# Optimization experiments

Measured on AMD Instinct MI355X. Metric: run time of the kernel, lower is better.

The kernel has to match this reference:

```python
import jax, jax.numpy as jnp
import numpy as np

VX = 1.0 / 3.2
VY = 1.0 / 3.2
X_MIN, Y_MIN = -40.0, -20.0
NX, NY = 256, 256  # grid: (40-(-40))/VX, (60-(-20))/VY
X_OFF = VX / 2.0 + X_MIN
Y_OFF = VY / 2.0 + Y_MIN


def setup_inputs() -> dict:
    key = jax.random.key(0)
    ks = jax.random.split(key, 14)
    B = 8
    Ma, Pa, Ca = 60000, 20, 5
    Mr, Pr, Cr = 80000, 32, 3
    Da, Dr, Co = 64, 64, 32
    voxels_agent = jax.random.normal(ks[0], (Ma, Pa, Ca), jnp.float32)
    coors_agent = jnp.stack([
        jax.random.randint(ks[1], (Ma,), 0, B),
        jax.random.randint(ks[2], (Ma,), 0, NY),
        jax.random.randint(ks[3], (Ma,), 0, NX)], axis=-1).astype(jnp.int32)
    num_points_agent = jax.random.randint(ks[4], (Ma,), 1, Pa + 1).astype(jnp.int32)
    voxels_rg = jax.random.normal(ks[5], (Mr, Pr, Cr), jnp.float32)
    coors_rg = jnp.stack([
        jax.random.randint(ks[6], (Mr,), 0, B),
        jax.random.randint(ks[7], (Mr,), 0, NY),
        jax.random.randint(ks[8], (Mr,), 0, NX)], axis=-1).astype(jnp.int32)
    num_points_rg = jax.random.randint(ks[9], (Mr,), 1, Pr + 1).astype(jnp.int32)
    w_agent = 0.02 * jax.random.normal(ks[10], (Ca + 5, Da), jnp.float32)
    b_agent = jnp.zeros((Da,), jnp.float32)
    w_rg = 0.02 * jax.random.normal(ks[11], (Cr + 5, Dr), jnp.float32)
    b_rg = jnp.zeros((Dr,), jnp.float32)
    conv_w = 0.02 * jax.random.normal(ks[12], (3, 3, Da + Dr, Co), jnp.float32)
    conv_b = jnp.zeros((Co,), jnp.float32)
    return dict(voxels_agent=voxels_agent, coors_agent=coors_agent,
                num_points_agent=num_points_agent, voxels_rg=voxels_rg,
                coors_rg=coors_rg, num_points_rg=num_points_rg,
                w_agent=w_agent, b_agent=b_agent, w_rg=w_rg, b_rg=b_rg,
                conv_w=conv_w, conv_b=conv_b, batch_size=B)


def _pillar_vfe(voxels, coors, num_points, W, b):
    # voxels [M,P,C]; coors [M,3]=(batch,y,x); num_points [M]
    M, P, C = voxels.shape
    mask = (jnp.arange(P)[None, :] < num_points[:, None]).astype(voxels.dtype)[..., None]  # [M,P,1]
    npts = jnp.maximum(num_points, 1).astype(voxels.dtype)[:, None, None]
    xyz = voxels[..., :3]
    mean = jnp.sum(xyz * mask, axis=1, keepdims=True) / npts          # pillar cluster mean
    f_cluster = xyz - mean                                            # [M,P,3]
    cx = coors[:, 2].astype(voxels.dtype)[:, None]
    cy = coors[:, 1].astype(voxels.dtype)[:, None]
    f_cx = voxels[..., 0] - (cx * VX + X_OFF)                         # offset from pillar center
    f_cy = voxels[..., 1] - (cy * VY + Y_OFF)
    feats = jnp.concatenate([voxels, f_cluster,
                             jnp.stack([f_cx, f_cy], axis=-1)], axis=-1) * mask  # [M,P,C+5]
    h = jax.nn.relu(feats @ W + b)                                    # [M,P,D]
    return jnp.max(h * mask, axis=1)                                  # [M,D]


def _scatter(feats, coors, B):
    # scatter pillar features into dense BEV canvas [B,NY,NX,D]
    D = feats.shape[1]
    idx = coors[:, 0] * (NY * NX) + coors[:, 1] * NX + coors[:, 2]
    canvas = jnp.zeros((B * NY * NX, D), feats.dtype).at[idx].set(feats)
    return canvas.reshape(B, NY, NX, D)


def reference(voxels_agent, coors_agent, num_points_agent, voxels_rg, coors_rg,
              num_points_rg, w_agent, b_agent, w_rg, b_rg, conv_w, conv_b,
              batch_size):
    pa = _pillar_vfe(voxels_agent, coors_agent, num_points_agent, w_agent, b_agent)
    ca = _scatter(pa, coors_agent, batch_size)
    pr = _pillar_vfe(voxels_rg, coors_rg, num_points_rg, w_rg, b_rg)
    cr = _scatter(pr, coors_rg, batch_size)
    x = jnp.concatenate([ca, cr], axis=-1)                            # [B,NY,NX,128] NHWC
    y = jax.lax.conv_general_dilated(x, conv_w, (1, 1), 'SAME',
                                     dimension_numbers=('NHWC', 'HWIO', 'NHWC'))
    return y + conv_b                                                 # [B,NY,NX,32]
```

## Files before the change

kernel.cpp:

```cpp
#include <hip/hip_runtime.h>
#include <hip/hip_bf16.h>

#define MA 60000
#define PA 20
#define CA 5
#define MR 80000
#define PR 32
#define CR 3
#define NXg 256
#define NYg 256
#define NB 8
#define NCELL (NB * NYg * NXg)

typedef __bf16 bf16x8 __attribute__((ext_vector_type(8)));
typedef float  f32x4  __attribute__((ext_vector_type(4)));
typedef float  f4     __attribute__((ext_vector_type(4)));
typedef float  f2     __attribute__((ext_vector_type(2)));

__device__ __forceinline__ unsigned short f2bf(float f) {
    unsigned int u = __float_as_uint(f);
    u += 0x7fffu + ((u >> 16) & 1u);
    return (unsigned short)(u >> 16);
}

__global__ void __launch_bounds__(256) prep_kernel(const float* __restrict__ conv_w,
                                                   unsigned short* __restrict__ bp) {
    int i = blockIdx.x * 256 + threadIdx.x;
    int j    = i & 7;
    int lane = (i >> 3) & 63;
    int nt   = (i >> 9) & 1;
    int kk   = (i >> 10) & 3;
    int tap  = i >> 12;
    int n = nt * 16 + (lane & 15);
    int k = kk * 32 + (lane >> 4) * 8 + j;
    bp[i] = f2bf(conv_w[(tap * 128 + k) * 32 + n]);
}

template <int CIN, int CF, int PMAX, int PMAXp>
__device__ __forceinline__ void vfe_body(
    int bid, const float* __restrict__ vox, const int* __restrict__ coors,
    const int* __restrict__ npts, const float* __restrict__ W,
    const float* __restrict__ bias, unsigned short* __restrict__ feat,
    int* __restrict__ win, int M, int which, f4* sq)
{
    constexpr int PC   = PMAX * CIN;
    constexpr int SR   = PMAXp * CIN;
    constexpr int SR4  = SR / 4;
    constexpr int PP4  = PMAXp / 4;
    constexpr int CPP  = PMAX / 4;
    constexpr int NP   = 32;

    float* sf = (float*)sq;
    int tid  = threadIdx.x;
    int wv   = tid >> 6;
    int lane = tid & 63;
    int base = bid * NP;
    int cnt  = M - base; cnt = cnt > NP ? NP : cnt;

    {
        const f4* gv = (const f4*)vox + (size_t)base * (PC / 4);
        int totc = cnt * CPP;
        for (int c0 = tid; c0 < totc; c0 += 128) {
            int p = c0 / CPP;
            int g = c0 - p * CPP;
            const f4* src = gv + c0 * CIN;
            f4 q[CIN];
#pragma unroll
            for (int t = 0; t < CIN; ++t) q[t] = src[t];
            float* dst = sf + p * SR + g * 4;
#pragma unroll
            for (int cch = 0; cch < CIN; ++cch) {
                f4 w;
#pragma unroll
                for (int j = 0; j < 4; ++j) {
                    int e = j * CIN + cch;
                    w[j] = q[e >> 2][e & 3];
                }
                *(f4*)(dst + cch * PMAXp) = w;
            }
        }
    }

    float wc[CF];
#pragma unroll
    for (int c = 0; c < CF; ++c) wc[c] = W[c * 64 + lane];
    float bd = bias[lane];
    f2 we2[CIN];
    we2[0] = (f2){wc[0] + wc[CIN + 0] + wc[CIN + 3], wc[0] + wc[CIN + 0] + wc[CIN + 3]};
    we2[1] = (f2){wc[1] + wc[CIN + 1] + wc[CIN + 4], wc[1] + wc[CIN + 1] + wc[CIN + 4]};
    we2[2] = (f2){wc[2] + wc[CIN + 2], wc[2] + wc[CIN + 2]};
#pragma unroll
    for (int c = 3; c < CIN; ++c) we2[c] = (f2){wc[c], wc[c]};

    __syncthreads();

    if (tid < cnt) {
        int np = npts[base + tid];
        np = np < 1 ? 1 : (np > PMAX ? PMAX : np);
        int np4 = (np + 3) & ~3;
        float v0[CIN];
#pragma unroll
        for (int c = 0; c < CIN; ++c) v0[c] = sf[tid * SR + c * PMAXp];
        for (int p = np; p < np4; ++p)
#pragma unroll
            for (int c = 0; c < CIN; ++c)
                sf[tid * SR + c * PMAXp + p] = v0[c];
    }
    __syncthreads();

    int np_n = 1, cb_n = 0, cy_n = 0, cx_n = 0;
    if (wv < cnt) {
        np_n = npts[base + wv];
        cb_n = coors[(base + wv) * 3 + 0];
        cy_n = coors[(base + wv) * 3 + 1];
        cx_n = coors[(base + wv) * 3 + 2];
    }

    for (int pi = wv; pi < cnt; pi += 2) {
        int np = np_n, cb = cb_n, cy = cy_n, cx = cx_n;
        int pn = pi + 2;
        if (pn < cnt) {
            np_n = npts[base + pn];
            cb_n = coors[(base + pn) * 3 + 0];
            cy_n = coors[(base + pn) * 3 + 1];
            cx_n = coors[(base + pn) * 3 + 2];
        }
        np = np < 1 ? 1 : (np > PMAX ? PMAX : np);
        int nblk = (np + 3) >> 2;
        float kf = (float)(nblk * 4 - np);

        const f4* pf4 = sq + pi * SR4;
        const float* pf = sf + pi * SR;
        float x0 = pf[0], y0 = pf[PMAXp], z0 = pf[2 * PMAXp];

        f2 sx2 = {0.f, 0.f}, sy2 = {0.f, 0.f}, sz2 = {0.f, 0.f};
        f2 b2  = {-1e30f, -1e30f};

        for (int g = 0; g < nblk; ++g) {
            f4 v[CIN];
#pragma unroll
            for (int c = 0; c < CIN; ++c) v[c] = pf4[c * PP4 + g];
#pragma unroll
            for (int j = 0; j < 2; ++j) {
                f2 x2 = (f2){v[0][2*j], v[0][2*j+1]};
                f2 y2 = (f2){v[1][2*j], v[1][2*j+1]};
                f2 z2 = (f2){v[2][2*j], v[2][2*j+1]};
                sx2 += x2; sy2 += y2; sz2 += z2;
                f2 d2 = x2 * we2[0] + y2 * we2[1] + z2 * we2[2];
#pragma unroll
                for (int c = 3; c < CIN; ++c) {
                    f2 e2 = (f2){v[c][2*j], v[c][2*j+1]};
                    d2 += e2 * we2[c];
                }
                b2 = __builtin_elementwise_max(b2, d2);
            }
        }

        float sx = sx2[0] + sx2[1] - kf * x0;
        float sy = sy2[0] + sy2[1] - kf * y0;
        float sz = sz2[0] + sz2[1] - kf * z0;
        float sbest = fmaxf(b2[0], b2[1]);

        float inv = 1.0f / (float)np;
        float mx = sx * inv, my = sy * inv, mz = sz * inv;
        float xo = (float)cx * 0.3125f + (-39.84375f);
        float yo = (float)cy * 0.3125f + (-19.84375f);
        float off = bd - (mx * wc[CIN + 0] + my * wc[CIN + 1] + mz * wc[CIN + 2])
                       - xo * wc[CIN + 3] - yo * wc[CIN + 4];
        float best = fmaxf(0.0f, sbest + off);

        feat[(size_t)(base + pi) * 64 + lane] = f2bf(best);

        if (lane == 0) {
            atomicMax(&win[((cb * NYg + cy) * NXg + cx) * 2 + which], base + pi);
        }
    }
}

__global__ void __launch_bounds__(128) vfe_all(
    const float* __restrict__ vox_a, const int* __restrict__ coor_a,
    const int* __restrict__ np_a, const float* __restrict__ w_a,
    const float* __restrict__ b_a, unsigned short* __restrict__ feat_a,
    const float* __restrict__ vox_r, const int* __restrict__ coor_r,
    const int* __restrict__ np_r, const float* __restrict__ w_r,
    const float* __restrict__ b_r, unsigned short* __restrict__ feat_r,
    int* __restrict__ win)
{
    __shared__ f4 sq[32 * 25];
    int bid = blockIdx.x;
    int g = bid / 7, r = bid - g * 7;
    if (r < 3)
        vfe_body<CA, CA + 5, PA, 20>(g * 3 + r, vox_a, coor_a, np_a, w_a, b_a,
                                     feat_a, win, MA, 0, sq);
    else
        vfe_body<CR, CR + 5, PR, 32>(g * 4 + (r - 3), vox_r, coor_r, np_r, w_r, b_r,
                                     feat_r, win, MR, 1, sq);
}

__global__ void __launch_bounds__(256) conv_kernel(
    const unsigned short* __restrict__ feat_a,
    const unsigned short* __restrict__ feat_r,
    const int2* __restrict__ win2,
    const unsigned short* __restrict__ bpack,
    const float* __restrict__ conv_b,
    float* __restrict__ out)
{
    __shared__ uint4 sA[396 * 5];

    int tid  = threadIdx.x;
    int lane = tid & 63;
    int wv   = tid >> 6;
    int bid  = blockIdx.x;
    int xg = bid & 3, yg = (bid >> 2) & 63, b = bid >> 8;
    int x0 = xg * 64, y0 = yg * 4;
    int mrow = lane & 15, quad = lane >> 4;

    int wA[2] = {-1, -1}, wR[2] = {-1, -1};
#pragma unroll
    for (int r = 0; r < 2; ++r) {
        int cell = tid + r * 256;
        if (cell < 396) {
            int iy = cell / 66, ix = cell - iy * 66;
            int yy = y0 - 1 + iy, xx = x0 - 1 + ix;
            if ((unsigned)yy < 256u && (unsigned)xx < 256u) {
                int2 w2 = win2[(((b << 8) + yy) << 8) + xx];
                wA[r] = w2.x; wR[r] = w2.y;
            }
        }
    }

    f32x4 acc0[4], acc1[4];
#pragma unroll
    for (int mt = 0; mt < 4; ++mt) {
        acc0[mt] = (f32x4){0.f, 0.f, 0.f, 0.f};
        acc1[mt] = (f32x4){0.f, 0.f, 0.f, 0.f};
    }

#pragma unroll
    for (int ph = 0; ph < 4; ++ph) {
        const unsigned short* feat = (ph < 2) ? feat_a : feat_r;
        const int half = (ph & 1) * 32;

#pragma unroll
        for (int r = 0; r < 2; ++r) {
            int cell = tid + r * 256;
            if (cell < 396) {
                int w = (ph < 2) ? wA[r] : wR[r];
                uint4* dst = &sA[cell * 5];
                if (w >= 0) {
                    const uint4* src = (const uint4*)(feat + ((long)w << 6) + half);
                    dst[0] = src[0]; dst[1] = src[1];
                    dst[2] = src[2]; dst[3] = src[3];
                } else {
                    uint4 zz = {0, 0, 0, 0};
                    dst[0] = zz; dst[1] = zz; dst[2] = zz; dst[3] = zz;
                }
            }
        }
        __syncthreads();

#pragma unroll
        for (int tap = 0; tap < 9; ++tap) {
            const int dyo = tap / 3, dxo = tap % 3;
            const unsigned short* bp = bpack + tap * 4096 + ph * 1024 + lane * 8;
            bf16x8 bn0 = *(const bf16x8*)(bp);
            bf16x8 bn1 = *(const bf16x8*)(bp + 512);
            int iy = wv + dyo;
#pragma unroll
            for (int mt = 0; mt < 4; ++mt) {
                int ix = mt * 16 + mrow + dxo;
                bf16x8 a = *(const bf16x8*)(&sA[(iy * 66 + ix) * 5 + quad]);
                acc0[mt] = __builtin_amdgcn_mfma_f32_16x16x32_bf16(a, bn0, acc0[mt], 0, 0, 0);
                acc1[mt] = __builtin_amdgcn_mfma_f32_16x16x32_bf16(a, bn1, acc1[mt], 0, 0, 0);
            }
        }
        __syncthreads();
    }

    int col = lane & 15;
    float bias0 = conv_b[col];
    float bias1 = conv_b[col + 16];
    int cellbase = ((((b << 8) + y0 + wv)) << 8) + x0;
#pragma unroll
    for (int mt = 0; mt < 4; ++mt) {
#pragma unroll
        for (int r = 0; r < 4; ++r) {
            int cell = cellbase + mt * 16 + quad * 4 + r;
            float* o = out + (long)cell * 32;
            o[col]      = acc0[mt][r] + bias0;
            o[col + 16] = acc1[mt][r] + bias1;
        }
    }
}

extern "C" void kernel_launch(void* const* d_in, const int* in_sizes, int n_in,
                              void* d_out, int out_size, void* d_ws, size_t ws_size,
                              hipStream_t stream)
{
    const float* vox_a  = (const float*)d_in[0];
    const int*   coor_a = (const int*)d_in[1];
    const int*   np_a   = (const int*)d_in[2];
    const float* vox_r  = (const float*)d_in[3];
    const int*   coor_r = (const int*)d_in[4];
    const int*   np_r   = (const int*)d_in[5];
    const float* w_a    = (const float*)d_in[6];
    const float* b_a    = (const float*)d_in[7];
    const float* w_r    = (const float*)d_in[8];
    const float* b_r    = (const float*)d_in[9];
    const float* conv_w = (const float*)d_in[10];
    const float* conv_b = (const float*)d_in[11];
    float* out = (float*)d_out;

    char* ws = (char*)d_ws;
    unsigned short* feat_a = (unsigned short*)(ws);
    unsigned short* feat_r = (unsigned short*)(ws + 7680000);
    int* win               = (int*)(ws + 17920000);
    unsigned short* bpack  = (unsigned short*)(ws + 17920000 + 4194304);

    hipMemsetAsync(win, 0xFF, 2 * (size_t)NCELL * sizeof(int), stream);
    hipLaunchKernelGGL(prep_kernel, dim3(144), dim3(256), 0, stream,
                       conv_w, bpack);
    hipLaunchKernelGGL(vfe_all, dim3(MA / 32 + MR / 32), dim3(128), 0, stream,
                       vox_a, coor_a, np_a, w_a, b_a, feat_a,
                       vox_r, coor_r, np_r, w_r, b_r, feat_r, win);
    hipLaunchKernelGGL(conv_kernel, dim3(2048), dim3(256), 0, stream,
                       feat_a, feat_r, (const int2*)win, bpack, conv_b, out);
}
```

Measured before the change: 212.1 us.

## Restructure VFE to per-wave pillar groups with skipped padding loads and precomputed means

Each wavefront now independently processes 16 pillars in its own shared-memory slot, so the block-wide __syncthreads barriers go away and blocks grow to 256 threads. The global-to-LDS staging skips 4-point chunks beyond each pillar's point count, and each lane precomputes its pillar's cluster mean so the per-pillar feature loop no longer accumulates sums. In exchange each wave loops serially over 16 pillars instead of two waves sharing 32, and the wave-to-pillar mapping and slot sizing are new.

```diff
diff --git a/kernel.cpp b/kernel.cpp
--- a/kernel.cpp
+++ b/kernel.cpp
@@ -36,50 +36,27 @@
     bp[i] = f2bf(conv_w[(tap * 128 + k) * 32 + n]);
 }
 
-template <int CIN, int CF, int PMAX, int PMAXp>
-__device__ __forceinline__ void vfe_body(
-    int bid, const float* __restrict__ vox, const int* __restrict__ coors,
+template <int CIN, int CF, int PMAX, int PMAXp, int WSLOT>
+__device__ __forceinline__ void vfe_wave(
+    int wpid, const float* __restrict__ vox, const int* __restrict__ coors,
     const int* __restrict__ npts, const float* __restrict__ W,
     const float* __restrict__ bias, unsigned short* __restrict__ feat,
-    int* __restrict__ win, int M, int which, f4* sq)
+    int* __restrict__ win, int M, int which, float* __restrict__ ws)
 {
-    constexpr int PC   = PMAX * CIN;
-    constexpr int SR   = PMAXp * CIN;
-    constexpr int SR4  = SR / 4;
-    constexpr int PP4  = PMAXp / 4;
-    constexpr int CPP  = PMAX / 4;
-    constexpr int NP   = 32;
-
-    float* sf = (float*)sq;
-    int tid  = threadIdx.x;
-    int wv   = tid >> 6;
-    int lane = tid & 63;
-    int base = bid * NP;
-    int cnt  = M - base; cnt = cnt > NP ? NP : cnt;
-
-    {
-        const f4* gv = (const f4*)vox + (size_t)base * (PC / 4);
-        int totc = cnt * CPP;
-        for (int c0 = tid; c0 < totc; c0 += 128) {
-            int p = c0 / CPP;
-            int g = c0 - p * CPP;
-            const f4* src = gv + c0 * CIN;
-            f4 q[CIN];
-#pragma unroll
-            for (int t = 0; t < CIN; ++t) q[t] = src[t];
-            float* dst = sf + p * SR + g * 4;
-#pragma unroll
-            for (int cch = 0; cch < CIN; ++cch) {
-                f4 w;
-#pragma unroll
-                for (int j = 0; j < 4; ++j) {
-                    int e = j * CIN + cch;
-                    w[j] = q[e >> 2][e & 3];
-                }
-                *(f4*)(dst + cch * PMAXp) = w;
-            }
-        }
-    }
+    constexpr int SR    = PMAXp * CIN;
+    constexpr int SR4   = SR / 4;
+    constexpr int PP4   = PMAXp / 4;
+    constexpr int CPP   = PMAX / 4;
+    constexpr int MEANOFF = 16 * SR;
+    constexpr int CITER = (16 * CPP + 63) / 64;
+
+    int lane = threadIdx.x & 63;
+    int base = wpid * 16;
+    if (base >= M) return;
+    int cnt = M - base; cnt = cnt > 16 ? 16 : cnt;
+
+    f4* sq    = (f4*)ws;
+    f4* mean4 = (f4*)(ws + MEANOFF);
 
     float wc[CF];
 #pragma unroll
@@ -92,33 +69,73 @@
 #pragma unroll
     for (int c = 3; c < CIN; ++c) we2[c] = (f2){wc[c], wc[c]};
 
-    __syncthreads();
-
-    if (tid < cnt) {
-        int np = npts[base + tid];
+    {
+        const f4* gv = (const f4*)vox + (size_t)base * (CPP * CIN);
+        int totc = cnt * CPP;
+#pragma unroll
+        for (int it = 0; it < CITER; ++it) {
+            int c0 = it * 64 + lane;
+            if (c0 < totc) {
+                int p = c0 / CPP;
+                int g = c0 - p * CPP;
+                int npc = npts[base + p];
+                npc = npc < 1 ? 1 : (npc > PMAX ? PMAX : npc);
+                if (g * 4 < npc) {
+                    const f4* src = gv + c0 * CIN;
+                    f4 q[CIN];
+#pragma unroll
+                    for (int t = 0; t < CIN; ++t) q[t] = src[t];
+                    float* dst = (float*)sq + p * SR + g * 4;
+#pragma unroll
+                    for (int cch = 0; cch < CIN; ++cch) {
+                        f4 w;
+#pragma unroll
+                        for (int j = 0; j < 4; ++j) {
+                            int e = j * CIN + cch;
+                            w[j] = q[e >> 2][e & 3];
+                        }
+                        *(f4*)(dst + cch * PMAXp) = w;
+                    }
+                }
+            }
+        }
+    }
+
+    if (lane < cnt) {
+        int np = npts[base + lane];
         np = np < 1 ? 1 : (np > PMAX ? PMAX : np);
         int np4 = (np + 3) & ~3;
+        int nblk = np4 >> 2;
+        float* pb = (float*)sq + lane * SR;
         float v0[CIN];
 #pragma unroll
-        for (int c = 0; c < CIN; ++c) v0[c] = sf[tid * SR + c * PMAXp];
+        for (int c = 0; c < CIN; ++c) v0[c] = pb[c * PMAXp];
         for (int p = np; p < np4; ++p)
 #pragma unroll
-            for (int c = 0; c < CIN; ++c)
-                sf[tid * SR + c * PMAXp + p] = v0[c];
-    }
-    __syncthreads();
-
-    int np_n = 1, cb_n = 0, cy_n = 0, cx_n = 0;
-    if (wv < cnt) {
-        np_n = npts[base + wv];
-        cb_n = coors[(base + wv) * 3 + 0];
-        cy_n = coors[(base + wv) * 3 + 1];
-        cx_n = coors[(base + wv) * 3 + 2];
-    }
-
-    for (int pi = wv; pi < cnt; pi += 2) {
+            for (int c = 0; c < CIN; ++c) pb[c * PMAXp + p] = v0[c];
+        const f4* pb4 = (const f4*)pb;
+        f4 ax = {0.f,0.f,0.f,0.f}, ay = {0.f,0.f,0.f,0.f}, az = {0.f,0.f,0.f,0.f};
+        for (int g = 0; g < nblk; ++g) {
+            ax += pb4[0 * PP4 + g];
+            ay += pb4[1 * PP4 + g];
+            az += pb4[2 * PP4 + g];
+        }
+        float kf = (float)(np4 - np);
+        float sx = (ax[0] + ax[1]) + (ax[2] + ax[3]) - kf * v0[0];
+        float sy = (ay[0] + ay[1]) + (ay[2] + ay[3]) - kf * v0[1];
+        float sz = (az[0] + az[1]) + (az[2] + az[3]) - kf * v0[2];
+        float inv = 1.0f / (float)np;
+        mean4[lane] = (f4){sx * inv, sy * inv, sz * inv, 0.0f};
+    }
+
+    int np_n = npts[base];
+    int cb_n = coors[base * 3 + 0];
+    int cy_n = coors[base * 3 + 1];
+    int cx_n = coors[base * 3 + 2];
+
+    for (int pi = 0; pi < cnt; ++pi) {
         int np = np_n, cb = cb_n, cy = cy_n, cx = cx_n;
-        int pn = pi + 2;
+        int pn = pi + 1;
         if (pn < cnt) {
             np_n = npts[base + pn];
             cb_n = coors[(base + pn) * 3 + 0];
@@ -127,14 +144,10 @@
         }
         np = np < 1 ? 1 : (np > PMAX ? PMAX : np);
         int nblk = (np + 3) >> 2;
-        float kf = (float)(nblk * 4 - np);
-
+
+        f4 m4 = mean4[pi];
         const f4* pf4 = sq + pi * SR4;
-        const float* pf = sf + pi * SR;
-        float x0 = pf[0], y0 = pf[PMAXp], z0 = pf[2 * PMAXp];
-
-        f2 sx2 = {0.f, 0.f}, sy2 = {0.f, 0.f}, sz2 = {0.f, 0.f};
-        f2 b2  = {-1e30f, -1e30f};
+        f2 b2 = {-1e30f, -1e30f};
 
         for (int g = 0; g < nblk; ++g) {
             f4 v[CIN];
@@ -142,30 +155,20 @@
             for (int c = 0; c < CIN; ++c) v[c] = pf4[c * PP4 + g];
 #pragma unroll
             for (int j = 0; j < 2; ++j) {
-                f2 x2 = (f2){v[0][2*j], v[0][2*j+1]};
-                f2 y2 = (f2){v[1][2*j], v[1][2*j+1]};
-                f2 z2 = (f2){v[2][2*j], v[2][2*j+1]};
-                sx2 += x2; sy2 += y2; sz2 += z2;
-                f2 d2 = x2 * we2[0] + y2 * we2[1] + z2 * we2[2];
-#pragma unroll
-                for (int c = 3; c < CIN; ++c) {
-                    f2 e2 = (f2){v[c][2*j], v[c][2*j+1]};
-                    d2 += e2 * we2[c];
-                }
+                f2 d2 = (f2){v[0][2*j], v[0][2*j+1]} * we2[0]
+                      + (f2){v[1][2*j], v[1][2*j+1]} * we2[1]
+                      + (f2){v[2][2*j], v[2][2*j+1]} * we2[2];
+#pragma unroll
+                for (int c = 3; c < CIN; ++c)
+                    d2 += (f2){v[c][2*j], v[c][2*j+1]} * we2[c];
                 b2 = __builtin_elementwise_max(b2, d2);
             }
         }
 
-        float sx = sx2[0] + sx2[1] - kf * x0;
-        float sy = sy2[0] + sy2[1] - kf * y0;
-        float sz = sz2[0] + sz2[1] - kf * z0;
         float sbest = fmaxf(b2[0], b2[1]);
-
-        float inv = 1.0f / (float)np;
-        float mx = sx * inv, my = sy * inv, mz = sz * inv;
         float xo = (float)cx * 0.3125f + (-39.84375f);
         float yo = (float)cy * 0.3125f + (-19.84375f);
-        float off = bd - (mx * wc[CIN + 0] + my * wc[CIN + 1] + mz * wc[CIN + 2])
+        float off = bd - (m4[0] * wc[CIN + 0] + m4[1] * wc[CIN + 1] + m4[2] * wc[CIN + 2])
                        - xo * wc[CIN + 3] - yo * wc[CIN + 4];
         float best = fmaxf(0.0f, sbest + off);
 
@@ -177,7 +180,7 @@
     }
 }
 
-__global__ void __launch_bounds__(128) vfe_all(
+__global__ void __launch_bounds__(256, 6) vfe_all(
     const float* __restrict__ vox_a, const int* __restrict__ coor_a,
     const int* __restrict__ np_a, const float* __restrict__ w_a,
     const float* __restrict__ b_a, unsigned short* __restrict__ feat_a,
@@ -186,15 +189,18 @@
     const float* __restrict__ b_r, unsigned short* __restrict__ feat_r,
     int* __restrict__ win)
 {
-    __shared__ f4 sq[32 * 25];
-    int bid = blockIdx.x;
-    int g = bid / 7, r = bid - g * 7;
-    if (r < 3)
-        vfe_body<CA, CA + 5, PA, 20>(g * 3 + r, vox_a, coor_a, np_a, w_a, b_a,
-                                     feat_a, win, MA, 0, sq);
+    constexpr int WSLOT = 1664;
+    __shared__ float smem[4 * WSLOT];
+    int wv = threadIdx.x >> 6;
+    int w  = blockIdx.x * 4 + wv;
+    int g7 = w / 7, r7 = w - g7 * 7;
+    float* ws = smem + wv * WSLOT;
+    if (r7 < 3)
+        vfe_wave<CA, CA + 5, PA, 20, WSLOT>(g7 * 3 + r7, vox_a, coor_a, np_a,
+                                            w_a, b_a, feat_a, win, MA, 0, ws);
     else
-        vfe_body<CR, CR + 5, PR, 32>(g * 4 + (r - 3), vox_r, coor_r, np_r, w_r, b_r,
-                                     feat_r, win, MR, 1, sq);
+        vfe_wave<CR, CR + 5, PR, 32, WSLOT>(g7 * 4 + (r7 - 3), vox_r, coor_r, np_r,
+                                            w_r, b_r, feat_r, win, MR, 1, ws);
 }
 
 __global__ void __launch_bounds__(256) conv_kernel(
@@ -320,7 +326,7 @@
     hipMemsetAsync(win, 0xFF, 2 * (size_t)NCELL * sizeof(int), stream);
     hipLaunchKernelGGL(prep_kernel, dim3(144), dim3(256), 0, stream,
                        conv_w, bpack);
-    hipLaunchKernelGGL(vfe_all, dim3(MA / 32 + MR / 32), dim3(128), 0, stream,
+    hipLaunchKernelGGL(vfe_all, dim3((3750 + 5000 + 3) / 4), dim3(256), 0, stream,
                        vox_a, coor_a, np_a, w_a, b_a, feat_a,
                        vox_r, coor_r, np_r, w_r, b_r, feat_r, win);
     hipLaunchKernelGGL(conv_kernel, dim3(2048), dim3(256), 0, stream,
```

Result: faster. 198.7 us (-6.3%).
